# Optimization experiments

Hardware: AMD Instinct MI355X
Metric: run time of the kernel (lower is better)

## Reference

```python
import jax, jax.numpy as jnp
import numpy as np

B, S, P, D, L = 8, 224, 14, 512, 6
NPS = S // P            # 16 patches per side
N = NPS * NPS           # 256 tokens
G = L - 1               # 5 feedforward groups
H = D * 4
TOKEN_ATTEND_SELF_VALUE = -0.0005


def setup_inputs() -> dict:
    key = jax.random.key(0)
    k = jax.random.split(key, 8)
    s = 0.02
    f = jnp.float32
    return {
        "img": jax.random.normal(k[0], (B, 3, S, S), f),
        "W_patch": jax.random.normal(k[1], (P * P * 3, D), f) * s,
        "b_patch": jnp.zeros((D,), f),
        "pos_emb": jax.random.normal(k[2], (N, D), f) * s,
        "init_levels": jax.random.normal(k[3], (L, D), f),
        "bu_W1": jax.random.normal(k[4], (G, D, H), f) * s,
        "bu_b1": jnp.zeros((G, H), f),
        "bu_W2": jax.random.normal(k[5], (G, H, D), f) * s,
        "bu_b2": jnp.zeros((G, D), f),
        "td_W1": jax.random.normal(k[6], (G, D, H), f) * s,
        "td_b1": jnp.zeros((G, H), f),
        "td_W2": jax.random.normal(k[7], (G, H, D), f) * s,
        "td_b2": jnp.zeros((G, D), f),
        "iters": 12,
    }


def _grouped_ff(x, W1, b1, W2, b2):
    # x: [b, n, G, d]; grouped 1x1 conv == independent per-level MLP
    h = jax.nn.gelu(jnp.einsum('bnld,ldh->bnlh', x, W1) + b1, approximate=False)
    return jnp.einsum('bnlh,lhd->bnld', h, W2) + b2


def _consensus(levels):
    # levels: [b, n, L, d]; q = levels, k = l2-normalized levels, v = levels
    d = levels.shape[-1]
    norm = jnp.maximum(jnp.linalg.norm(levels, axis=-1, keepdims=True), 1e-12)
    k = levels / norm
    sim = jnp.einsum('bild,bjld->blij', levels, k) * (d ** -0.5)
    n = levels.shape[1]
    eye = jnp.eye(n, dtype=bool)[None, None]
    sim = jnp.where(eye, TOKEN_ATTEND_SELF_VALUE, sim)  # attend_self=False
    attn = jax.nn.softmax(sim, axis=-1)
    return jnp.einsum('blij,bjld->bild', attn, levels)


def _forward(img, W_patch, b_patch, pos_emb, init_levels,
             bu_W1, bu_b1, bu_W2, bu_b2, td_W1, td_b1, td_W2, td_b2, iters):
    b = img.shape[0]
    # 'b c (h p1) (w p2) -> b (h w) (p1 p2 c)'
    x = img.reshape(b, 3, NPS, P, NPS, P).transpose(0, 2, 4, 3, 5, 1).reshape(b, N, P * P * 3)
    tokens = x @ W_patch + b_patch                  # [b, n, d]
    bottom = tokens[:, :, None, :]                  # [b, n, 1, d]
    levels = jnp.broadcast_to(init_levels, (b, N, L, D)).astype(img.dtype)
    pos = pos_emb[None, :, None, :]
    contrib = jnp.array([4.0] * (L - 1) + [3.0], jnp.float32).reshape(1, 1, L, 1)

    def step(lv, _):
        lw = jnp.concatenate([bottom, lv], axis=-2)                 # [b, n, L+1, d]
        bu = _grouped_ff(lw[..., 1:-1, :], bu_W1, bu_b1, bu_W2, bu_b2)
        td = _grouped_ff(lw[..., 2:, :] + pos, td_W1, td_b1, td_W2, td_b2)
        bu = jnp.concatenate([bottom, bu], axis=-2)                 # [b, n, L, d]
        td = jnp.pad(td, ((0, 0), (0, 0), (0, 1), (0, 0)))          # [b, n, L, d]
        cons = _consensus(lv)
        new = (lv + bu + td + cons) / contrib
        return new, None

    levels, _ = jax.lax.scan(step, levels, None, length=iters)
    return levels


def reference(img, W_patch, b_patch, pos_emb, init_levels,
              bu_W1, bu_b1, bu_W2, bu_b2, td_W1, td_b1, td_W2, td_b2, iters):
    return _forward(img, W_patch, b_patch, pos_emb, init_levels,
                    bu_W1, bu_b1, bu_W2, bu_b2, td_W1, td_b1, td_W2, td_b2, iters)
```

## Files before the change

kernel.cpp:

```cpp
#include <hip/hip_runtime.h>
#include <math.h>

#define L6 6

typedef __attribute__((ext_vector_type(8))) short bf16x8;
typedef __attribute__((ext_vector_type(4))) float f32x4;

#define SH_W_GRP   2097152ull
#define SH_A_TDOFF 10485760ull

__device__ __forceinline__ float gelu_exact(float x) {
  return 0.5f * x * (1.0f + erff(x * 0.70710678118654752f));
}

__device__ __forceinline__ unsigned short bf16_rn(float x) {
  unsigned u = __float_as_uint(x);
  unsigned r = u + 0x7FFFu + ((u >> 16) & 1u);
  return (unsigned short)(r >> 16);
}
__device__ __forceinline__ float bf16_f(unsigned short h) {
  return __uint_as_float(((unsigned)h) << 16);
}
__device__ __forceinline__ void split2(float x, unsigned short* h, unsigned short* l) {
  unsigned short hh = bf16_rn(x);
  *h = hh;
  *l = bf16_rn(x - bf16_f(hh));
}
__device__ __forceinline__ int4 pack8(const unsigned short* v) {
  return make_int4((int)((unsigned)v[0] | ((unsigned)v[1] << 16)),
                   (int)((unsigned)v[2] | ((unsigned)v[3] << 16)),
                   (int)((unsigned)v[4] | ((unsigned)v[5] << 16)),
                   (int)((unsigned)v[6] | ((unsigned)v[7] << 16)));
}

__device__ __forceinline__ void gload16(const void* g, void* l) {
  __builtin_amdgcn_global_load_lds(
      (const __attribute__((address_space(1))) void*)g,
      (__attribute__((address_space(3))) void*)l, 16, 0, 0);
}

__global__ __launch_bounds__(256) void patch_embed(
    const float* __restrict__ img, const float* __restrict__ Wp,
    const float* __restrict__ bp, float* __restrict__ tokens)
{
  __shared__ float xs[588];
  const int bn = blockIdx.x;
  const int b = bn >> 8, n = bn & 255;
  const int i = n >> 4, j = n & 15;
  for (int k = threadIdx.x; k < 588; k += 256) {
    int c = k % 3;
    int t = k / 3;
    int pc = t % 14;
    int pr = t / 14;
    xs[k] = img[(((size_t)(b * 3 + c) * 224) + (i * 14 + pr)) * 224 + (j * 14 + pc)];
  }
  __syncthreads();
  const int d0 = threadIdx.x, d1 = threadIdx.x + 256;
  float a0 = 0.f, a1 = 0.f;
  for (int k = 0; k < 588; ++k) {
    float x = xs[k];
    a0 = fmaf(x, Wp[(size_t)k * 512 + d0], a0);
    a1 = fmaf(x, Wp[(size_t)k * 512 + d1], a1);
  }
  tokens[(size_t)bn * 512 + d0] = a0 + bp[d0];
  tokens[(size_t)bn * 512 + d1] = a1 + bp[d1];
}

__global__ __launch_bounds__(256) void init_lv_kernel(
    const float* __restrict__ initl, float* __restrict__ lv)
{
  int f = blockIdx.x * 256 + threadIdx.x;
  int d4 = f & 127;
  int l = (f >> 15) % 6;
  float4 v = *(const float4*)(initl + (size_t)l * 512 + d4 * 4);
  *(float4*)(lv + (size_t)f * 4) = v;
}

__global__ __launch_bounds__(256) void norm0_k(
    const float* __restrict__ lv, float* __restrict__ invn)
{
  int bl = blockIdx.x;
  int n = threadIdx.x;
  const float* row = lv + ((size_t)bl * 256 + n) * 512;
  float ss = 0.f;
  for (int k = 0; k < 512; k += 4) {
    float4 v = *(const float4*)(row + k);
    ss = fmaf(v.x, v.x, ss);
    ss = fmaf(v.y, v.y, ss);
    ss = fmaf(v.z, v.z, ss);
    ss = fmaf(v.w, v.w, ss);
  }
  invn[(size_t)bl * 256 + n] = 1.0f / fmaxf(sqrtf(ss), 1e-12f);
}

__global__ __launch_bounds__(256) void pack_w(
    const float* __restrict__ src, short* __restrict__ dst, int KT, int NT)
{
  int sidx = blockIdx.x * 256 + threadIdx.x;
  int slot = sidx & 511;
  int blk = sidx >> 9;
  int kt = blk % KT;
  int rest = blk / KT;
  int nt = rest % NT;
  int g = rest / NT;
  int f = slot >> 6, lane = slot & 63;
  int N = NT * 128, K = KT * 32;
  int n = nt * 128 + f * 16 + (lane & 15);
  int k0 = kt * 32 + (lane >> 4) * 8;
  const float* s = src + ((size_t)g * K + k0) * N + n;
  unsigned short hi[8], lo[8];
#pragma unroll
  for (int j = 0; j < 8; ++j) split2(s[(size_t)j * N], &hi[j], &lo[j]);
  short* d = dst + (size_t)blk * 8192 + slot * 8;
  *(int4*)d = pack8(hi);
  *(int4*)(d + 4096) = pack8(lo);
}

__global__ __launch_bounds__(256) void pack_A(
    const float* __restrict__ lv, const float* __restrict__ pos,
    short* __restrict__ Abu, short* __restrict__ Atd)
{
  const int bx = blockIdx.x;
  const int lg = bx >> 8, mt = (bx >> 4) & 15, kt = bx & 15;
  const size_t blk = (size_t)bx * 8192;
#pragma unroll
  for (int ss = 0; ss < 2; ++ss) {
    int s = threadIdx.x + ss * 256;
    int f = s >> 6, l = s & 63;
    int m = mt * 128 + (f << 4) + (l & 15);
    int b = m >> 8, n = m & 255;
    int d = kt * 32 + ((l >> 4) << 3);
    const float* pbu = lv + ((size_t)(b * L6 + lg) * 256 + n) * 512 + d;
    const float* ptd = lv + ((size_t)(b * L6 + lg + 1) * 256 + n) * 512 + d;
    const float* pp = pos + (size_t)n * 512 + d;
    float4 u0 = *(const float4*)pbu;
    float4 u1 = *(const float4*)(pbu + 4);
    float xv[8] = {u0.x, u0.y, u0.z, u0.w, u1.x, u1.y, u1.z, u1.w};
    unsigned short hi[8], lo[8];
#pragma unroll
    for (int j = 0; j < 8; ++j) split2(xv[j], &hi[j], &lo[j]);
    *(int4*)(Abu + blk + s * 8) = pack8(hi);
    *(int4*)(Abu + blk + 4096 + s * 8) = pack8(lo);
    float4 v0 = *(const float4*)ptd;
    float4 v1 = *(const float4*)(ptd + 4);
    float4 p0 = *(const float4*)pp;
    float4 p1 = *(const float4*)(pp + 4);
    float yv[8] = {v0.x + p0.x, v0.y + p0.y, v0.z + p0.z, v0.w + p0.w,
                   v1.x + p1.x, v1.y + p1.y, v1.z + p1.z, v1.w + p1.w};
#pragma unroll
    for (int j = 0; j < 8; ++j) split2(yv[j], &hi[j], &lo[j]);
    *(int4*)(Atd + blk + s * 8) = pack8(hi);
    *(int4*)(Atd + blk + 4096 + s * 8) = pack8(lo);
  }
}

__global__ __launch_bounds__(256, 3) void ff1_k(
    const short* __restrict__ Wa, const short* __restrict__ Ap,
    const float* __restrict__ b1, short* __restrict__ hpk)
{
  const int per_x = gridDim.x >> 3;
  const int gid = (blockIdx.x & 7) * per_x + (blockIdx.x >> 3);
  const int tt = gid & 15;
  const int tile = gid >> 4;
  const int ht = tile & 15;
  const int z = tile >> 4;
  const int tid = threadIdx.x, lane = tid & 63, w = tid >> 6;
  const int wm = (w >> 1) * 64, wn = (w & 1) * 64;
  const short* ga = Wa + (size_t)(z * 16 + ht) * 16 * 8192 + (wm << 5) + lane * 8;
  const short* gb = Ap + (size_t)(z * 16 + tt) * 16 * 8192 + (wn << 5) + lane * 8;

  f32x4 acc[4][4];
#pragma unroll
  for (int i = 0; i < 4; ++i)
#pragma unroll
    for (int j = 0; j < 4; ++j) acc[i][j] = (f32x4)(0.0f);

  for (int kt = 0; kt < 16; ++kt) {
    const short* pa = ga + (size_t)kt * 8192;
    const short* pb = gb + (size_t)kt * 8192;
    bf16x8 ah[4], al[4], bh[4], bl[4];
#pragma unroll
    for (int i = 0; i < 4; ++i) {
      ah[i] = *(const bf16x8*)(pa + i * 512);
      al[i] = *(const bf16x8*)(pa + 4096 + i * 512);
    }
#pragma unroll
    for (int j = 0; j < 4; ++j) {
      bh[j] = *(const bf16x8*)(pb + j * 512);
      bl[j] = *(const bf16x8*)(pb + 4096 + j * 512);
    }
#pragma unroll
    for (int j = 0; j < 4; ++j)
#pragma unroll
      for (int i = 0; i < 4; ++i)
        acc[i][j] = __builtin_amdgcn_mfma_f32_16x16x32_bf16(
            ah[i], bh[j], acc[i][j], 0, 0, 0);
#pragma unroll
    for (int j = 0; j < 4; ++j)
#pragma unroll
      for (int i = 0; i < 4; ++i)
        acc[i][j] = __builtin_amdgcn_mfma_f32_16x16x32_bf16(
            al[i], bh[j], acc[i][j], 0, 0, 0);
#pragma unroll
    for (int j = 0; j < 4; ++j)
#pragma unroll
      for (int i = 0; i < 4; ++i)
        acc[i][j] = __builtin_amdgcn_mfma_f32_16x16x32_bf16(
            ah[i], bl[j], acc[i][j], 0, 0, 0);
  }

  const int q = lane >> 4, t = lane & 15;
  const float* b1g = b1 + (size_t)z * 2048;
#pragma unroll
  for (int i = 0; i < 4; ++i) {
    int Hb = ht * 128 + wm + i * 16 + q * 4;
    float4 bv = *(const float4*)(b1g + Hb);
    float bb[4] = {bv.x, bv.y, bv.z, bv.w};
    int kt2 = Hb >> 5;
    int g2 = (Hb >> 3) & 3;
    int jb = Hb & 7;
    size_t blkbase = ((size_t)(z * 16 + tt) * 64 + kt2) * 4096;
#pragma unroll
    for (int j = 0; j < 4; ++j) {
      int f2 = (wn >> 4) + j;
      size_t off = blkbase + (size_t)(f2 * 64 + g2 * 16 + t) * 8 + jb;
      unsigned short hi[4];
#pragma unroll
      for (int r = 0; r < 4; ++r)
        hi[r] = bf16_rn(gelu_exact(acc[i][j][r] + bb[r]));
      *(uint2*)(hpk + off) =
          make_uint2((unsigned)hi[0] | ((unsigned)hi[1] << 16),
                     (unsigned)hi[2] | ((unsigned)hi[3] << 16));
    }
  }
}

__global__ __launch_bounds__(256, 3) void attn_k(
    const float* __restrict__ lv, const short* __restrict__ Apk,
    const float* __restrict__ invn, float* __restrict__ attnb)
{
  __shared__ __align__(16) short Bhi[8192];
  __shared__ __align__(16) short Blo[8192];
  __shared__ float scL[256];
  __shared__ float red[32][4];
  const int a = blockIdx.x;
  const int s = a >> 3;
  const int b = a & 7;
  const int l = s >> 3;
  const int bl = b * 6 + l;
  const int i0 = (s & 7) * 32;
  const float* base = lv + (size_t)bl * 131072;
  const int tid = threadIdx.x, lane = tid & 63, w = tid >> 6;
  const int q = lane >> 4, c = lane & 15;

  scL[tid] = invn[(size_t)bl * 256 + tid];

  f32x4 acc[2][4];
#pragma unroll
  for (int i = 0; i < 2; ++i)
#pragma unroll
    for (int j = 0; j < 4; ++j) acc[i][j] = (f32x4)(0.0f);

  const short* src0 = Apk + ((size_t)(l * 16 + 2 * b) * 16) * 8192;
  const short* src1 = Apk + ((size_t)(l * 16 + 2 * b + 1) * 16) * 8192;

  for (int kt = 0; kt < 16; ++kt) {
    __syncthreads();
    if (l < 5) {
      const char* p0 = (const char*)(src0 + (size_t)kt * 8192);
      const char* p1 = (const char*)(src1 + (size_t)kt * 8192);
      gload16(p0 + tid * 16,         (char*)Bhi + tid * 16);
      gload16(p0 + 4096 + tid * 16,  (char*)Bhi + 4096 + tid * 16);
      gload16(p0 + 8192 + tid * 16,  (char*)Blo + tid * 16);
      gload16(p0 + 12288 + tid * 16, (char*)Blo + 4096 + tid * 16);
      gload16(p1 + tid * 16,         (char*)Bhi + 8192 + tid * 16);
      gload16(p1 + 4096 + tid * 16,  (char*)Bhi + 12288 + tid * 16);
      gload16(p1 + 8192 + tid * 16,  (char*)Blo + 8192 + tid * 16);
      gload16(p1 + 12288 + tid * 16, (char*)Blo + 12288 + tid * 16);
    } else {
      const int k0 = kt * 32;
#pragma unroll
      for (int it = 0; it < 8; ++it) {
        int f = it * 256 + tid;
        int j = f >> 3, c4 = f & 7;
        float4 v = *(const float4*)(base + (size_t)j * 512 + k0 + c4 * 4);
        unsigned short hi[4], lo[4];
        split2(v.x, &hi[0], &lo[0]);
        split2(v.y, &hi[1], &lo[1]);
        split2(v.z, &hi[2], &lo[2]);
        split2(v.w, &hi[3], &lo[3]);
        int fg = j >> 4;
        int la = (c4 >> 1) * 16 + (j & 15);
        int half = (c4 & 1) * 4;
        *(uint2*)&Bhi[fg * 512 + la * 8 + half] =
            make_uint2((unsigned)hi[0] | ((unsigned)hi[1] << 16),
                       (unsigned)hi[2] | ((unsigned)hi[3] << 16));
        *(uint2*)&Blo[fg * 512 + la * 8 + half] =
            make_uint2((unsigned)lo[0] | ((unsigned)lo[1] << 16),
                       (unsigned)lo[2] | ((unsigned)lo[3] << 16));
      }
    }
    __syncthreads();
    bf16x8 ah[2], al[2], bh[4], blv[4];
#pragma unroll
    for (int i = 0; i < 2; ++i) {
      int fg = (i0 >> 4) + i;
      ah[i] = *(const bf16x8*)&Bhi[fg * 512 + lane * 8];
      al[i] = *(const bf16x8*)&Blo[fg * 512 + lane * 8];
    }
#pragma unroll
    for (int j = 0; j < 4; ++j) {
      int fg = w * 4 + j;
      bh[j] = *(const bf16x8*)&Bhi[fg * 512 + lane * 8];
      blv[j] = *(const bf16x8*)&Blo[fg * 512 + lane * 8];
    }
#pragma unroll
    for (int j = 0; j < 4; ++j)
#pragma unroll
      for (int i = 0; i < 2; ++i)
        acc[i][j] = __builtin_amdgcn_mfma_f32_16x16x32_bf16(
            ah[i], bh[j], acc[i][j], 0, 0, 0);
#pragma unroll
    for (int j = 0; j < 4; ++j)
#pragma unroll
      for (int i = 0; i < 2; ++i)
        acc[i][j] = __builtin_amdgcn_mfma_f32_16x16x32_bf16(
            al[i], bh[j], acc[i][j], 0, 0, 0);
#pragma unroll
    for (int j = 0; j < 4; ++j)
#pragma unroll
      for (int i = 0; i < 2; ++i)
        acc[i][j] = __builtin_amdgcn_mfma_f32_16x16x32_bf16(
            ah[i], blv[j], acc[i][j], 0, 0, 0);
  }
  __syncthreads();

  const float rs = 0.04419417382415922f;
#pragma unroll
  for (int ai = 0; ai < 2; ++ai)
#pragma unroll
    for (int bj = 0; bj < 4; ++bj)
#pragma unroll
      for (int r = 0; r < 4; ++r) {
        int i = i0 + ai * 16 + q * 4 + r;
        int j = w * 64 + bj * 16 + c;
        float sv = acc[ai][bj][r] * scL[j] * rs;
        if (j == i) sv = -0.0005f;
        acc[ai][bj][r] = sv;
      }
  float mx[2][4];
#pragma unroll
  for (int ai = 0; ai < 2; ++ai)
#pragma unroll
    for (int r = 0; r < 4; ++r) {
      float m = fmaxf(fmaxf(acc[ai][0][r], acc[ai][1][r]),
                      fmaxf(acc[ai][2][r], acc[ai][3][r]));
      m = fmaxf(m, __shfl_xor(m, 1));
      m = fmaxf(m, __shfl_xor(m, 2));
      m = fmaxf(m, __shfl_xor(m, 4));
      m = fmaxf(m, __shfl_xor(m, 8));
      mx[ai][r] = m;
    }
  if (c == 0) {
#pragma unroll
    for (int ai = 0; ai < 2; ++ai)
#pragma unroll
      for (int r = 0; r < 4; ++r) red[ai * 16 + q * 4 + r][w] = mx[ai][r];
  }
  __syncthreads();
#pragma unroll
  for (int ai = 0; ai < 2; ++ai)
#pragma unroll
    for (int r = 0; r < 4; ++r) {
      int row = ai * 16 + q * 4 + r;
      mx[ai][r] = fmaxf(fmaxf(red[row][0], red[row][1]),
                        fmaxf(red[row][2], red[row][3]));
    }
  __syncthreads();
  float sm[2][4];
#pragma unroll
  for (int ai = 0; ai < 2; ++ai)
#pragma unroll
    for (int r = 0; r < 4; ++r) {
      float t = 0.f;
#pragma unroll
      for (int bj = 0; bj < 4; ++bj) {
        float e = expf(acc[ai][bj][r] - mx[ai][r]);
        acc[ai][bj][r] = e;
        t += e;
      }
      t += __shfl_xor(t, 1);
      t += __shfl_xor(t, 2);
      t += __shfl_xor(t, 4);
      t += __shfl_xor(t, 8);
      sm[ai][r] = t;
    }
  if (c == 0) {
#pragma unroll
    for (int ai = 0; ai < 2; ++ai)
#pragma unroll
      for (int r = 0; r < 4; ++r) red[ai * 16 + q * 4 + r][w] = sm[ai][r];
  }
  __syncthreads();
  float* ob = attnb + (size_t)bl * 65536;
#pragma unroll
  for (int ai = 0; ai < 2; ++ai)
#pragma unroll
    for (int r = 0; r < 4; ++r) {
      int row = ai * 16 + q * 4 + r;
      float S = red[row][0] + red[row][1] + red[row][2] + red[row][3];
      float inv = 1.0f / S;
      int i = i0 + row;
#pragma unroll
      for (int bj = 0; bj < 4; ++bj) {
        int j = w * 64 + bj * 16 + c;
        ob[(size_t)i * 256 + j] = acc[ai][bj][r] * inv;
      }
    }
}

__global__ __launch_bounds__(256) void cons_k(
    const float* __restrict__ attnb, const float* __restrict__ lv,
    float* __restrict__ accum)
{
  __shared__ __align__(16) char smemraw[25088];
  const int a = blockIdx.x;
  const int s = a >> 3;
  const int bl = (a & 7) * 6 + (s >> 4);
  const int tile = s & 15;
  int it0 = (tile >> 2) * 64;
  int dt0 = (tile & 3) * 128;
  const float* A = attnb + (size_t)bl * 65536;
  const float* Bm = lv + (size_t)bl * 131072;
  float (*Ast)[68] = (float(*)[68])smemraw;
  float (*Bs)[128] = (float(*)[128])(smemraw + 8704);
  const int tid = threadIdx.x;
  const int ty = tid >> 4, tx = tid & 15;
  float acc[4][8];
#pragma unroll
  for (int i = 0; i < 4; ++i)
#pragma unroll
    for (int j = 0; j < 8; ++j) acc[i][j] = 0.f;

  for (int k0 = 0; k0 < 256; k0 += 32) {
#pragma unroll
    for (int it = 0; it < 2; ++it) {
      int f = it * 256 + tid;
      int r = f >> 3, c4 = f & 7;
      float4 v = *(const float4*)(A + (size_t)(it0 + r) * 256 + k0 + c4 * 4);
      Ast[c4 * 4 + 0][r] = v.x;
      Ast[c4 * 4 + 1][r] = v.y;
      Ast[c4 * 4 + 2][r] = v.z;
      Ast[c4 * 4 + 3][r] = v.w;
    }
#pragma unroll
    for (int it = 0; it < 4; ++it) {
      int kr = (tid >> 5) + it * 8;
      int c4 = tid & 31;
      *(float4*)&Bs[kr][c4 * 4] =
          *(const float4*)(Bm + (size_t)(k0 + kr) * 512 + dt0 + c4 * 4);
    }
    __syncthreads();
#pragma unroll 8
    for (int k = 0; k < 32; ++k) {
      float4 av = *(const float4*)&Ast[k][ty * 4];
      float4 b0 = *(const float4*)&Bs[k][tx * 4];
      float4 b1 = *(const float4*)&Bs[k][64 + tx * 4];
      float avv[4] = {av.x, av.y, av.z, av.w};
      float bv[8] = {b0.x, b0.y, b0.z, b0.w, b1.x, b1.y, b1.z, b1.w};
#pragma unroll
      for (int i = 0; i < 4; ++i)
#pragma unroll
        for (int j = 0; j < 8; ++j)
          acc[i][j] = fmaf(avv[i], bv[j], acc[i][j]);
    }
    __syncthreads();
  }
#pragma unroll
  for (int ii = 0; ii < 4; ++ii) {
    int i = it0 + ty * 4 + ii;
    float* arow = accum + (size_t)bl * 131072 + (size_t)i * 512 + dt0;
#pragma unroll
    for (int j = 0; j < 4; ++j) arow[tx * 4 + j] += acc[ii][j];
#pragma unroll
    for (int j = 0; j < 4; ++j) arow[64 + tx * 4 + j] += acc[ii][4 + j];
  }
}

__global__ __launch_bounds__(256, 4) void mfma_ff2(
    const short* __restrict__ hpk, const short* __restrict__ Wb,
    const float* __restrict__ b2, const float* __restrict__ lv,
    const float* __restrict__ tokens, float* __restrict__ accum,
    int olvbase, int emode)
{
  const int per_x = gridDim.x >> 3;
  const int gid = (blockIdx.x & 7) * per_x + (blockIdx.x >> 3);
  const int nt2 = gid & 3;
  const int tile = gid >> 2;
  const int mt2 = tile & 31;
  const int z = tile >> 5;

  __shared__ __align__(16) short SA[2048];
  __shared__ __align__(16) short SB[8192];
  const int tid = threadIdx.x, lane = tid & 63, w = tid >> 6;
  const int wm = (w >> 1) * 32, wn = (w & 1) * 64;
  const short* gaBase = hpk + (size_t)(z * 16 + (mt2 >> 1)) * 64 * 4096
                        + (size_t)(mt2 & 1) * 2048;
  const short* gb = Wb + (size_t)(z * 4 + nt2) * 64 * 8192;

  f32x4 acc[2][4];
#pragma unroll
  for (int i = 0; i < 2; ++i)
#pragma unroll
    for (int j = 0; j < 4; ++j) acc[i][j] = (f32x4)(0.0f);

  for (int kt = 0; kt < 64; ++kt) {
    __syncthreads();
    const char* pa = (const char*)(gaBase + (size_t)kt * 4096);
    const char* pb = (const char*)(gb + (size_t)kt * 8192);
    gload16(pa + w * 1024 + lane * 16, (char*)SA + w * 1024);
#pragma unroll
    for (int c = 0; c < 4; ++c)
      gload16(pb + w * 4096 + c * 1024 + lane * 16,
              (char*)SB + w * 4096 + c * 1024);
    __syncthreads();
    bf16x8 ah[2];
#pragma unroll
    for (int i = 0; i < 2; ++i) {
      int f = (wm >> 4) + i;
      ah[i] = *(const bf16x8*)&SA[f * 512 + lane * 8];
    }
#pragma unroll
    for (int jp = 0; jp < 2; ++jp) {
      bf16x8 bh[2], bl[2];
#pragma unroll
      for (int j2 = 0; j2 < 2; ++j2) {
        int f = (wn >> 4) + jp * 2 + j2;
        bh[j2] = *(const bf16x8*)&SB[f * 512 + lane * 8];
        bl[j2] = *(const bf16x8*)&SB[4096 + f * 512 + lane * 8];
      }
#pragma unroll
      for (int j2 = 0; j2 < 2; ++j2)
#pragma unroll
        for (int i = 0; i < 2; ++i)
          acc[i][jp * 2 + j2] = __builtin_amdgcn_mfma_f32_16x16x32_bf16(
              ah[i], bh[j2], acc[i][jp * 2 + j2], 0, 0, 0);
#pragma unroll
      for (int j2 = 0; j2 < 2; ++j2)
#pragma unroll
        for (int i = 0; i < 2; ++i)
          acc[i][jp * 2 + j2] = __builtin_amdgcn_mfma_f32_16x16x32_bf16(
              ah[i], bl[j2], acc[i][jp * 2 + j2], 0, 0, 0);
    }
  }

  const int q = lane >> 4, t = lane & 15;
  const float* b2g = b2 + (size_t)z * 512;
  const int level = olvbase + z;
#pragma unroll
  for (int i = 0; i < 2; ++i) {
#pragma unroll
    for (int r = 0; r < 4; ++r) {
      int m = mt2 * 64 + wm + i * 16 + q * 4 + r;
      int b = m >> 8, n = m & 255;
      size_t rowoff = ((size_t)(b * L6 + level) * 256 + n) * 512;
      float* arow = accum + rowoff;
      const float* lrow = lv + rowoff;
      const float* trow = tokens + (size_t)m * 512;
#pragma unroll
      for (int j = 0; j < 4; ++j) {
        int col = nt2 * 128 + wn + j * 16 + t;
        float v = acc[i][j][r] + b2g[col];
        if (emode == 0)                       arow[col] = lrow[col] + v;
        else if (level == 0)                  arow[col] = lrow[col] + trow[col] + v;
        else                                  arow[col] += v;
      }
    }
  }
}

__global__ __launch_bounds__(256) void combine3(
    const float* __restrict__ accum, const float* __restrict__ pos,
    float* __restrict__ lv_out, short* __restrict__ Abu,
    short* __restrict__ Atd, float* __restrict__ invn,
    float* __restrict__ dout, int last)
{
  int t = blockIdx.x * 256 + threadIdx.x;
  int d8 = t & 63;
  int n = (t >> 6) & 255;
  int v = t >> 14;
  int l = v % 6, b = v / 6;
  int bn = (b << 8) | n;
  size_t idx = ((size_t)v * 256 + n) * 512 + d8 * 8;
  float4 a0 = *(const float4*)(accum + idx);
  float4 a1 = *(const float4*)(accum + idx + 4);
  float sc = (l == 5) ? (1.0f / 3.0f) : 0.25f;
  float r[8];
  r[0] = a0.x * sc; r[1] = a0.y * sc; r[2] = a0.z * sc; r[3] = a0.w * sc;
  r[4] = a1.x * sc; r[5] = a1.y * sc; r[6] = a1.z * sc; r[7] = a1.w * sc;
  *(float4*)(lv_out + idx) = make_float4(r[0], r[1], r[2], r[3]);
  *(float4*)(lv_out + idx + 4) = make_float4(r[4], r[5], r[6], r[7]);
  if (last) {
    float* dp = dout + ((size_t)bn * 6 + l) * 512 + d8 * 8;
    *(float4*)dp = make_float4(r[0], r[1], r[2], r[3]);
    *(float4*)(dp + 4) = make_float4(r[4], r[5], r[6], r[7]);
  }
  {
    float s8 = 0.f;
#pragma unroll
    for (int j = 0; j < 8; ++j) s8 = fmaf(r[j], r[j], s8);
#pragma unroll
    for (int o = 1; o < 64; o <<= 1) s8 += __shfl_xor(s8, o);
    if (d8 == 0) invn[(size_t)v * 256 + n] = 1.0f / fmaxf(sqrtf(s8), 1e-12f);
  }
  int m = bn;
  int mt = m >> 7;
  int kt = d8 >> 2;
  int s = (((m & 127) >> 4) << 6) | (((d8 & 3) << 4) | (m & 15));
  unsigned short hi[8], lo[8];
  if (l < 5) {
    size_t blk = ((size_t)(l * 16 + mt) * 16 + kt) * 8192;
#pragma unroll
    for (int j = 0; j < 8; ++j) split2(r[j], &hi[j], &lo[j]);
    *(int4*)(Abu + blk + s * 8) = pack8(hi);
    *(int4*)(Abu + blk + 4096 + s * 8) = pack8(lo);
  }
  if (l >= 1) {
    const float* pp = pos + (size_t)n * 512 + d8 * 8;
    float4 p0 = *(const float4*)pp;
    float4 p1 = *(const float4*)(pp + 4);
    float y[8] = {r[0] + p0.x, r[1] + p0.y, r[2] + p0.z, r[3] + p0.w,
                  r[4] + p1.x, r[5] + p1.y, r[6] + p1.z, r[7] + p1.w};
    size_t blk = ((size_t)((l - 1) * 16 + mt) * 16 + kt) * 8192;
#pragma unroll
    for (int j = 0; j < 8; ++j) split2(y[j], &hi[j], &lo[j]);
    *(int4*)(Atd + blk + s * 8) = pack8(hi);
    *(int4*)(Atd + blk + 4096 + s * 8) = pack8(lo);
  }
}

extern "C" void kernel_launch(void* const* d_in, const int* in_sizes, int n_in,
                              void* d_out, int out_size, void* d_ws, size_t ws_size,
                              hipStream_t stream)
{
  const float* img   = (const float*)d_in[0];
  const float* Wp    = (const float*)d_in[1];
  const float* bp    = (const float*)d_in[2];
  const float* pos   = (const float*)d_in[3];
  const float* initl = (const float*)d_in[4];
  const float* buW1  = (const float*)d_in[5];
  const float* bub1  = (const float*)d_in[6];
  const float* buW2  = (const float*)d_in[7];
  const float* bub2  = (const float*)d_in[8];
  const float* tdW1  = (const float*)d_in[9];
  const float* tdb1  = (const float*)d_in[10];
  const float* tdW2  = (const float*)d_in[11];
  const float* tdb2  = (const float*)d_in[12];

  float* ws = (float*)d_ws;
  const size_t LV = (size_t)8 * 6 * 256 * 512;
  float* lv     = ws;
  float* tokens = lv + LV;
  float* accum  = tokens + 1048576ull;
  short* W1all  = (short*)(accum + LV);
  short* W2all  = W1all + 20971520ull;
  short* Apk    = W2all + 20971520ull;
  short* hall   = Apk + 20971520ull;
  float* invn   = (float*)(hall + 41943040ull);

  float* attnb = (float*)(hall + 20971520ull);
  float* dout  = (float*)d_out;

  pack_w<<<2560, 256, 0, stream>>>(buW1, W1all, 16, 16);
  pack_w<<<2560, 256, 0, stream>>>(tdW1, W1all + 5 * SH_W_GRP, 16, 16);
  pack_w<<<2560, 256, 0, stream>>>(buW2, W2all, 64, 4);
  pack_w<<<2560, 256, 0, stream>>>(tdW2, W2all + 5 * SH_W_GRP, 64, 4);

  patch_embed<<<2048, 256, 0, stream>>>(img, Wp, bp, tokens);
  init_lv_kernel<<<6144, 256, 0, stream>>>(initl, lv);
  norm0_k<<<48, 256, 0, stream>>>(lv, invn);
  pack_A<<<1280, 256, 0, stream>>>(lv, pos, Apk, Apk + SH_A_TDOFF);

  for (int it = 0; it < 12; ++it) {
    ff1_k<<<1280, 256, 0, stream>>>(W1all, Apk, bub1, hall);
    mfma_ff2<<<640, 256, 0, stream>>>(hall, W2all, bub2, lv, tokens, accum, 1, 0);
    ff1_k<<<1280, 256, 0, stream>>>(W1all + 5 * SH_W_GRP, Apk + SH_A_TDOFF,
                                    tdb1, hall);
    mfma_ff2<<<640, 256, 0, stream>>>(hall, W2all + 5 * SH_W_GRP, tdb2, lv,
                                      tokens, accum, 0, 1);
    attn_k<<<384, 256, 0, stream>>>(lv, Apk, invn, attnb);
    cons_k<<<768, 256, 0, stream>>>(attnb, lv, accum);
    combine3<<<3072, 256, 0, stream>>>(accum, pos, lv, Apk, Apk + SH_A_TDOFF,
                                       invn, dout, it == 11 ? 1 : 0);
  }
}
```

Before: 4.163 ms.

## Co-schedule independent FF2/FF1 and FF2/attention work in merged kernel launches

Merges bottom-up FF2 with top-down FF1, and top-down FF2 with the attention-score kernel, into single launches whose blocks branch on blockIdx. These pairs are independent, so running them together fills the GPU and cuts launch gaps and tail effects. Separate hidden buffers for the bu and td paths let them coexist, and attnb now aliases the bu hidden buffer, which is dead by then. The merged kernels share one LDS allocation sized for the larger body, and ff2 runs at 3 blocks per CU instead of 4. Patch embedding also splits K across two thread halves with float4 weight loads.

```diff
diff --git a/kernel.cpp b/kernel.cpp
--- a/kernel.cpp
+++ b/kernel.cpp
@@ -44,6 +44,7 @@
     const float* __restrict__ bp, float* __restrict__ tokens)
 {
   __shared__ float xs[588];
+  __shared__ float part[128][4];
   const int bn = blockIdx.x;
   const int b = bn >> 8, n = bn & 255;
   const int i = n >> 4, j = n & 15;
@@ -55,15 +56,29 @@
     xs[k] = img[(((size_t)(b * 3 + c) * 224) + (i * 14 + pr)) * 224 + (j * 14 + pc)];
   }
   __syncthreads();
-  const int d0 = threadIdx.x, d1 = threadIdx.x + 256;
-  float a0 = 0.f, a1 = 0.f;
-  for (int k = 0; k < 588; ++k) {
+  const int kh = threadIdx.x >> 7;
+  const int dq = threadIdx.x & 127;
+  const int d0 = dq * 4;
+  float a0 = 0.f, a1 = 0.f, a2 = 0.f, a3 = 0.f;
+  const int kbeg = kh * 294, kend = kbeg + 294;
+  for (int k = kbeg; k < kend; ++k) {
     float x = xs[k];
-    a0 = fmaf(x, Wp[(size_t)k * 512 + d0], a0);
-    a1 = fmaf(x, Wp[(size_t)k * 512 + d1], a1);
-  }
-  tokens[(size_t)bn * 512 + d0] = a0 + bp[d0];
-  tokens[(size_t)bn * 512 + d1] = a1 + bp[d1];
+    float4 wv = *(const float4*)(Wp + (size_t)k * 512 + d0);
+    a0 = fmaf(x, wv.x, a0);
+    a1 = fmaf(x, wv.y, a1);
+    a2 = fmaf(x, wv.z, a2);
+    a3 = fmaf(x, wv.w, a3);
+  }
+  if (kh == 0) {
+    part[dq][0] = a0; part[dq][1] = a1; part[dq][2] = a2; part[dq][3] = a3;
+  }
+  __syncthreads();
+  if (kh == 1) {
+    float4 bv = *(const float4*)(bp + d0);
+    float4 o = make_float4(part[dq][0] + a0 + bv.x, part[dq][1] + a1 + bv.y,
+                           part[dq][2] + a2 + bv.z, part[dq][3] + a3 + bv.w);
+    *(float4*)(tokens + (size_t)bn * 512 + d0) = o;
+  }
 }
 
 __global__ __launch_bounds__(256) void init_lv_kernel(
@@ -154,12 +169,10 @@
   }
 }
 
-__global__ __launch_bounds__(256, 3) void ff1_k(
+__device__ __forceinline__ void ff1_body(
     const short* __restrict__ Wa, const short* __restrict__ Ap,
-    const float* __restrict__ b1, short* __restrict__ hpk)
-{
-  const int per_x = gridDim.x >> 3;
-  const int gid = (blockIdx.x & 7) * per_x + (blockIdx.x >> 3);
+    const float* __restrict__ b1, short* __restrict__ hpk, int gid)
+{
   const int tt = gid & 15;
   const int tile = gid >> 4;
   const int ht = tile & 15;
@@ -235,15 +248,104 @@
   }
 }
 
-__global__ __launch_bounds__(256, 3) void attn_k(
-    const float* __restrict__ lv, const short* __restrict__ Apk,
-    const float* __restrict__ invn, float* __restrict__ attnb)
-{
-  __shared__ __align__(16) short Bhi[8192];
-  __shared__ __align__(16) short Blo[8192];
-  __shared__ float scL[256];
-  __shared__ float red[32][4];
-  const int a = blockIdx.x;
+__device__ __forceinline__ void ff2_body(
+    char* smem, const short* __restrict__ hpk, const short* __restrict__ Wb,
+    const float* __restrict__ b2, const float* __restrict__ lv,
+    const float* __restrict__ tokens, float* __restrict__ accum,
+    int olvbase, int emode, int gid)
+{
+  short* SA = (short*)smem;
+  short* SB = (short*)(smem + 4096);
+  const int nt2 = gid & 3;
+  const int tile = gid >> 2;
+  const int mt2 = tile & 31;
+  const int z = tile >> 5;
+
+  const int tid = threadIdx.x, lane = tid & 63, w = tid >> 6;
+  const int wm = (w >> 1) * 32, wn = (w & 1) * 64;
+  const short* gaBase = hpk + (size_t)(z * 16 + (mt2 >> 1)) * 64 * 4096
+                        + (size_t)(mt2 & 1) * 2048;
+  const short* gb = Wb + (size_t)(z * 4 + nt2) * 64 * 8192;
+
+  f32x4 acc[2][4];
+#pragma unroll
+  for (int i = 0; i < 2; ++i)
+#pragma unroll
+    for (int j = 0; j < 4; ++j) acc[i][j] = (f32x4)(0.0f);
+
+  for (int kt = 0; kt < 64; ++kt) {
+    __syncthreads();
+    const char* pa = (const char*)(gaBase + (size_t)kt * 4096);
+    const char* pb = (const char*)(gb + (size_t)kt * 8192);
+    gload16(pa + w * 1024 + lane * 16, (char*)SA + w * 1024);
+#pragma unroll
+    for (int c = 0; c < 4; ++c)
+      gload16(pb + w * 4096 + c * 1024 + lane * 16,
+              (char*)SB + w * 4096 + c * 1024);
+    __syncthreads();
+    bf16x8 ah[2];
+#pragma unroll
+    for (int i = 0; i < 2; ++i) {
+      int f = (wm >> 4) + i;
+      ah[i] = *(const bf16x8*)&SA[f * 512 + lane * 8];
+    }
+#pragma unroll
+    for (int jp = 0; jp < 2; ++jp) {
+      bf16x8 bh[2], bl[2];
+#pragma unroll
+      for (int j2 = 0; j2 < 2; ++j2) {
+        int f = (wn >> 4) + jp * 2 + j2;
+        bh[j2] = *(const bf16x8*)&SB[f * 512 + lane * 8];
+        bl[j2] = *(const bf16x8*)&SB[4096 + f * 512 + lane * 8];
+      }
+#pragma unroll
+      for (int j2 = 0; j2 < 2; ++j2)
+#pragma unroll
+        for (int i = 0; i < 2; ++i)
+          acc[i][jp * 2 + j2] = __builtin_amdgcn_mfma_f32_16x16x32_bf16(
+              ah[i], bh[j2], acc[i][jp * 2 + j2], 0, 0, 0);
+#pragma unroll
+      for (int j2 = 0; j2 < 2; ++j2)
+#pragma unroll
+        for (int i = 0; i < 2; ++i)
+          acc[i][jp * 2 + j2] = __builtin_amdgcn_mfma_f32_16x16x32_bf16(
+              ah[i], bl[j2], acc[i][jp * 2 + j2], 0, 0, 0);
+    }
+  }
+
+  const int q = lane >> 4, t = lane & 15;
+  const float* b2g = b2 + (size_t)z * 512;
+  const int level = olvbase + z;
+#pragma unroll
+  for (int i = 0; i < 2; ++i) {
+#pragma unroll
+    for (int r = 0; r < 4; ++r) {
+      int m = mt2 * 64 + wm + i * 16 + q * 4 + r;
+      int b = m >> 8, n = m & 255;
+      size_t rowoff = ((size_t)(b * L6 + level) * 256 + n) * 512;
+      float* arow = accum + rowoff;
+      const float* lrow = lv + rowoff;
+      const float* trow = tokens + (size_t)m * 512;
+#pragma unroll
+      for (int j = 0; j < 4; ++j) {
+        int col = nt2 * 128 + wn + j * 16 + t;
+        float v = acc[i][j][r] + b2g[col];
+        if (emode == 0)                       arow[col] = lrow[col] + v;
+        else if (level == 0)                  arow[col] = lrow[col] + trow[col] + v;
+        else                                  arow[col] += v;
+      }
+    }
+  }
+}
+
+__device__ __forceinline__ void attn_body(
+    char* smem, const float* __restrict__ lv, const short* __restrict__ Apk,
+    const float* __restrict__ invn, float* __restrict__ attnb, int a)
+{
+  short* Bhi = (short*)smem;
+  short* Blo = (short*)(smem + 16384);
+  float* scL = (float*)(smem + 32768);
+  float (*red)[4] = (float(*)[4])(smem + 33792);
   const int s = a >> 3;
   const int b = a & 7;
   const int l = s >> 3;
@@ -419,6 +521,51 @@
     }
 }
 
+__global__ __launch_bounds__(256, 3) void ff1_k(
+    const short* __restrict__ Wa, const short* __restrict__ Ap,
+    const float* __restrict__ b1, short* __restrict__ hpk)
+{
+  const int per_x = gridDim.x >> 3;
+  const int gid = (blockIdx.x & 7) * per_x + (blockIdx.x >> 3);
+  ff1_body(Wa, Ap, b1, hpk, gid);
+}
+
+__global__ __launch_bounds__(256, 3) void k_ff2bu_ff1td(
+    const short* __restrict__ hallbu, const short* __restrict__ W2,
+    const float* __restrict__ bub2, const float* __restrict__ lv,
+    const float* __restrict__ tokens, float* __restrict__ accum,
+    const short* __restrict__ W1td, const short* __restrict__ Atd,
+    const float* __restrict__ tdb1, short* __restrict__ halltd)
+{
+  __shared__ __align__(16) char smem[20480];
+  if (blockIdx.x < 640) {
+    int bid = blockIdx.x;
+    int gid = (bid & 7) * 80 + (bid >> 3);
+    ff2_body(smem, hallbu, W2, bub2, lv, tokens, accum, 1, 0, gid);
+  } else {
+    int bid = blockIdx.x - 640;
+    int gid = (bid & 7) * 160 + (bid >> 3);
+    ff1_body(W1td, Atd, tdb1, halltd, gid);
+  }
+}
+
+__global__ __launch_bounds__(256, 3) void k_ff2td_attn(
+    const short* __restrict__ halltd, const short* __restrict__ W2td,
+    const float* __restrict__ tdb2, const float* __restrict__ lv,
+    const float* __restrict__ tokens, float* __restrict__ accum,
+    const short* __restrict__ Apk, const float* __restrict__ invn,
+    float* __restrict__ attnb)
+{
+  __shared__ __align__(16) char smem[34304];
+  if (blockIdx.x < 640) {
+    int bid = blockIdx.x;
+    int gid = (bid & 7) * 80 + (bid >> 3);
+    ff2_body(smem, halltd, W2td, tdb2, lv, tokens, accum, 0, 1, gid);
+  } else {
+    attn_body(smem, lv, Apk, invn, attnb, blockIdx.x - 640);
+  }
+}
+
 __global__ __launch_bounds__(256) void cons_k(
     const float* __restrict__ attnb, const float* __restrict__ lv,
     float* __restrict__ accum)
@@ -484,98 +631,6 @@
     for (int j = 0; j < 4; ++j) arow[tx * 4 + j] += acc[ii][j];
 #pragma unroll
     for (int j = 0; j < 4; ++j) arow[64 + tx * 4 + j] += acc[ii][4 + j];
-  }
-}
-
-__global__ __launch_bounds__(256, 4) void mfma_ff2(
-    const short* __restrict__ hpk, const short* __restrict__ Wb,
-    const float* __restrict__ b2, const float* __restrict__ lv,
-    const float* __restrict__ tokens, float* __restrict__ accum,
-    int olvbase, int emode)
-{
-  const int per_x = gridDim.x >> 3;
-  const int gid = (blockIdx.x & 7) * per_x + (blockIdx.x >> 3);
-  const int nt2 = gid & 3;
-  const int tile = gid >> 2;
-  const int mt2 = tile & 31;
-  const int z = tile >> 5;
-
-  __shared__ __align__(16) short SA[2048];
-  __shared__ __align__(16) short SB[8192];
-  const int tid = threadIdx.x, lane = tid & 63, w = tid >> 6;
-  const int wm = (w >> 1) * 32, wn = (w & 1) * 64;
-  const short* gaBase = hpk + (size_t)(z * 16 + (mt2 >> 1)) * 64 * 4096
-                        + (size_t)(mt2 & 1) * 2048;
-  const short* gb = Wb + (size_t)(z * 4 + nt2) * 64 * 8192;
-
-  f32x4 acc[2][4];
-#pragma unroll
-  for (int i = 0; i < 2; ++i)
-#pragma unroll
-    for (int j = 0; j < 4; ++j) acc[i][j] = (f32x4)(0.0f);
-
-  for (int kt = 0; kt < 64; ++kt) {
-    __syncthreads();
-    const char* pa = (const char*)(gaBase + (size_t)kt * 4096);
-    const char* pb = (const char*)(gb + (size_t)kt * 8192);
-    gload16(pa + w * 1024 + lane * 16, (char*)SA + w * 1024);
-#pragma unroll
-    for (int c = 0; c < 4; ++c)
-      gload16(pb + w * 4096 + c * 1024 + lane * 16,
-              (char*)SB + w * 4096 + c * 1024);
-    __syncthreads();
-    bf16x8 ah[2];
-#pragma unroll
-    for (int i = 0; i < 2; ++i) {
-      int f = (wm >> 4) + i;
-      ah[i] = *(const bf16x8*)&SA[f * 512 + lane * 8];
-    }
-#pragma unroll
-    for (int jp = 0; jp < 2; ++jp) {
-      bf16x8 bh[2], bl[2];
-#pragma unroll
-      for (int j2 = 0; j2 < 2; ++j2) {
-        int f = (wn >> 4) + jp * 2 + j2;
-        bh[j2] = *(const bf16x8*)&SB[f * 512 + lane * 8];
-        bl[j2] = *(const bf16x8*)&SB[4096 + f * 512 + lane * 8];
-      }
-#pragma unroll
-      for (int j2 = 0; j2 < 2; ++j2)
-#pragma unroll
-        for (int i = 0; i < 2; ++i)
-          acc[i][jp * 2 + j2] = __builtin_amdgcn_mfma_f32_16x16x32_bf16(
-              ah[i], bh[j2], acc[i][jp * 2 + j2], 0, 0, 0);
-#pragma unroll
-      for (int j2 = 0; j2 < 2; ++j2)
-#pragma unroll
-        for (int i = 0; i < 2; ++i)
-          acc[i][jp * 2 + j2] = __builtin_amdgcn_mfma_f32_16x16x32_bf16(
-              ah[i], bl[j2], acc[i][jp * 2 + j2], 0, 0, 0);
-    }
-  }
-
-  const int q = lane >> 4, t = lane & 15;
-  const float* b2g = b2 + (size_t)z * 512;
-  const int level = olvbase + z;
-#pragma unroll
-  for (int i = 0; i < 2; ++i) {
-#pragma unroll
-    for (int r = 0; r < 4; ++r) {
-      int m = mt2 * 64 + wm + i * 16 + q * 4 + r;
-      int b = m >> 8, n = m & 255;
-      size_t rowoff = ((size_t)(b * L6 + level) * 256 + n) * 512;
-      float* arow = accum + rowoff;
-      const float* lrow = lv + rowoff;
-      const float* trow = tokens + (size_t)m * 512;
-#pragma unroll
-      for (int j = 0; j < 4; ++j) {
-        int col = nt2 * 128 + wn + j * 16 + t;
-        float v = acc[i][j][r] + b2g[col];
-        if (emode == 0)                       arow[col] = lrow[col] + v;
-        else if (level == 0)                  arow[col] = lrow[col] + trow[col] + v;
-        else                                  arow[col] += v;
-      }
-    }
   }
 }
 
@@ -665,10 +720,11 @@
   short* W1all  = (short*)(accum + LV);
   short* W2all  = W1all + 20971520ull;
   short* Apk    = W2all + 20971520ull;
-  short* hall   = Apk + 20971520ull;
-  float* invn   = (float*)(hall + 41943040ull);
-
-  float* attnb = (float*)(hall + 20971520ull);
+  short* hallbu = Apk + 20971520ull;
+  short* halltd = hallbu + 20971520ull;
+  float* invn   = (float*)(halltd + 20971520ull);
+
+  float* attnb = (float*)hallbu;
   float* dout  = (float*)d_out;
 
   pack_w<<<2560, 256, 0, stream>>>(buW1, W1all, 16, 16);
@@ -682,13 +738,13 @@
   pack_A<<<1280, 256, 0, stream>>>(lv, pos, Apk, Apk + SH_A_TDOFF);
 
   for (int it = 0; it < 12; ++it) {
-    ff1_k<<<1280, 256, 0, stream>>>(W1all, Apk, bub1, hall);
-    mfma_ff2<<<640, 256, 0, stream>>>(hall, W2all, bub2, lv, tokens, accum, 1, 0);
-    ff1_k<<<1280, 256, 0, stream>>>(W1all + 5 * SH_W_GRP, Apk + SH_A_TDOFF,
-                                    tdb1, hall);
-    mfma_ff2<<<640, 256, 0, stream>>>(hall, W2all + 5 * SH_W_GRP, tdb2, lv,
-                                      tokens, accum, 0, 1);
-    attn_k<<<384, 256, 0, stream>>>(lv, Apk, invn, attnb);
+    ff1_k<<<1280, 256, 0, stream>>>(W1all, Apk, bub1, hallbu);
+    k_ff2bu_ff1td<<<1920, 256, 0, stream>>>(
+        hallbu, W2all, bub2, lv, tokens, accum,
+        W1all + 5 * SH_W_GRP, Apk + SH_A_TDOFF, tdb1, halltd);
+    k_ff2td_attn<<<1024, 256, 0, stream>>>(
+        halltd, W2all + 5 * SH_W_GRP, tdb2, lv, tokens, accum,
+        Apk, invn, attnb);
     cons_k<<<768, 256, 0, stream>>>(attnb, lv, accum);
     combine3<<<3072, 256, 0, stream>>>(accum, pos, lv, Apk, Apk + SH_A_TDOFF,
                                        invn, dout, it == 11 ? 1 : 0);
```

Measured after the change: 3.915 ms. 6.0% less time.
